# Kernel optimization log

Hardware: AMD Instinct MI355X
Metric: run time of the kernel (lower is better)

Reference implementation:

```python
import jax, jax.numpy as jnp
import numpy as np
from jax import lax

BN_EPS = 1e-5


def _conv(x, w, b):
    # 3x3 conv, stride 1, padding 1 (SAME), NCHW/OIHW
    y = lax.conv_general_dilated(x, w, (1, 1), 'SAME',
                                 dimension_numbers=('NCHW', 'OIHW', 'NCHW'))
    return y + b[None, :, None, None]


def _bn(x, g, b, m, v):
    # eval-mode batchnorm with running stats
    scale = (g / jnp.sqrt(v + BN_EPS))[None, :, None, None]
    return (x - m[None, :, None, None]) * scale + b[None, :, None, None]


def _pool(x):
    # MaxPool2d(2,2), VALID (floor division of spatial dims)
    return lax.reduce_window(x, -jnp.inf, lax.max, (1, 1, 2, 2), (1, 1, 2, 2), 'VALID')


def _quantum(xq, qp):
    """Batched 5-qubit statevector sim of the PennyLane circuit.
    Wire i: RX(xq[:, i%2]) then RY(qp[i%2]); CNOT(0,1); CNOT(1,2); <Z0 Z1>.
    xq: [B, 32] (only first 2 features used). Returns [B] float32.
    """
    B = xq.shape[0]
    psi = jnp.zeros((B, 32), jnp.complex64).at[:, 0].set(1.0)
    for i in range(5):  # fixed tiny loop over wires
        a = xq[:, i % 2]          # [B] data angle
        th = qp[i % 2]            # scalar weight angle
        ca, sa = jnp.cos(a * 0.5), jnp.sin(a * 0.5)
        RX = jnp.stack([jnp.stack([ca, -1j * sa], -1),
                        jnp.stack([-1j * sa, ca], -1)], -2).astype(jnp.complex64)  # [B,2,2]
        cb, sb = jnp.cos(th * 0.5), jnp.sin(th * 0.5)
        RY = jnp.stack([jnp.stack([cb, -sb]), jnp.stack([sb, cb])]).astype(jnp.complex64)  # [2,2]
        U = jnp.einsum('ij,bjk->bik', RY, RX)  # [B,2,2] per-wire unitary
        psi = psi.reshape(B, 2 ** i, 2, 2 ** (4 - i))
        psi = jnp.einsum('bij,bajc->baic', U, psi).reshape(B, 32)
    psi = psi.reshape(B, 2, 2, 2, 2, 2)
    # CNOT(0,1): flip qubit 1 where qubit 0 == 1
    psi = psi.at[:, 1].set(psi[:, 1, ::-1])
    # CNOT(1,2): flip qubit 2 where qubit 1 == 1
    psi = psi.at[:, :, 1].set(psi[:, :, 1, ::-1])
    z01 = jnp.array([[1.0, -1.0], [-1.0, 1.0]], jnp.float32).reshape(1, 2, 2, 1, 1, 1)
    prob = jnp.real(psi) ** 2 + jnp.imag(psi) ** 2
    return jnp.sum(prob * z01, axis=(1, 2, 3, 4, 5))


def setup_inputs() -> dict:
    key = jax.random.key(0)
    ks = jax.random.split(key, 24)
    B = 8192
    s = 0.05
    d = {}
    d['x'] = jax.random.normal(ks[0], (B, 1, 28, 28), jnp.float32)
    d['conv1_w'] = jax.random.normal(ks[1], (64, 1, 3, 3), jnp.float32) * s
    d['conv1_b'] = jax.random.normal(ks[2], (64,), jnp.float32) * s
    d['conv2_w'] = jax.random.normal(ks[3], (128, 64, 3, 3), jnp.float32) * s
    d['conv2_b'] = jax.random.normal(ks[4], (128,), jnp.float32) * s
    d['conv3_w'] = jax.random.normal(ks[5], (256, 128, 3, 3), jnp.float32) * s
    d['conv3_b'] = jax.random.normal(ks[6], (256,), jnp.float32) * s
    for i, c in [(1, 64), (2, 128), (3, 256)]:
        d[f'bn{i}_g'] = jnp.ones((c,), jnp.float32)
        d[f'bn{i}_b'] = jnp.zeros((c,), jnp.float32)
        d[f'bn{i}_m'] = jax.random.normal(ks[6 + i], (c,), jnp.float32) * 0.1
        d[f'bn{i}_v'] = jax.random.uniform(ks[9 + i], (c,), jnp.float32, 0.5, 1.5)
    d['fc1_w'] = jax.random.normal(ks[13], (32, 256 * 3 * 3), jnp.float32) * s
    d['fc1_b'] = jax.random.normal(ks[14], (32,), jnp.float32) * s
    d['q_params'] = jax.random.uniform(ks[15], (8,), jnp.float32)
    d['fc2_w'] = jax.random.normal(ks[16], (128, 1), jnp.float32) * s
    d['fc2_b'] = jax.random.normal(ks[17], (128,), jnp.float32) * s
    d['fc3_w'] = jax.random.normal(ks[18], (2, 128), jnp.float32) * s
    d['fc3_b'] = jax.random.normal(ks[19], (2,), jnp.float32) * s
    return d


def reference(x, conv1_w, conv1_b, conv2_w, conv2_b, conv3_w, conv3_b,
              bn1_g, bn1_b, bn1_m, bn1_v, bn2_g, bn2_b, bn2_m, bn2_v,
              bn3_g, bn3_b, bn3_m, bn3_v, fc1_w, fc1_b, q_params,
              fc2_w, fc2_b, fc3_w, fc3_b):
    h = _pool(jax.nn.relu(_bn(_conv(x, conv1_w, conv1_b), bn1_g, bn1_b, bn1_m, bn1_v)))
    h = _pool(jax.nn.relu(_bn(_conv(h, conv2_w, conv2_b), bn2_g, bn2_b, bn2_m, bn2_v)))
    h = _pool(jax.nn.relu(_bn(_conv(h, conv3_w, conv3_b), bn3_g, bn3_b, bn3_m, bn3_v)))
    # dropout is identity in eval mode
    h = h.reshape(h.shape[0], -1)              # [B, 2304]
    h = h @ fc1_w.T + fc1_b                     # [B, 32]
    q = _quantum(h, q_params)[:, None]          # [B, 1]
    h = q @ fc2_w.T + fc2_b                     # [B, 128]
    logits = h @ fc3_w.T + fc3_b                # [B, 2]
    return jax.nn.log_softmax(logits, axis=1)
```

## Files before the change

kernel.cpp:

```cpp
#include <hip/hip_runtime.h>
#include <hip/hip_bf16.h>
#include <math.h>

typedef float f32x4 __attribute__((ext_vector_type(4)));
typedef float f32x2 __attribute__((ext_vector_type(2)));
typedef short s16x8 __attribute__((ext_vector_type(8)));

static const long long OFF_W2  = 0LL;
static const long long OFF_W3  = 147456LL;
static const long long OFF_AB1 = 737280LL;
static const long long OFF_AB2 = 737792LL;
static const long long OFF_AB3 = 738816LL;
static const long long OFF_Q   = 740864LL;

__device__ inline unsigned short f2bfu(float f) {
    __hip_bfloat16 h = __float2bfloat16(f);
    unsigned short u;
    __builtin_memcpy(&u, &h, 2);
    return u;
}

__global__ __launch_bounds__(256) void prep_k(
    const float* __restrict__ c2w, const float* __restrict__ c3w,
    const float* __restrict__ c1b, const float* __restrict__ g1, const float* __restrict__ b1,
    const float* __restrict__ m1, const float* __restrict__ v1,
    const float* __restrict__ c2b, const float* __restrict__ g2, const float* __restrict__ b2,
    const float* __restrict__ m2, const float* __restrict__ v2,
    const float* __restrict__ c3b, const float* __restrict__ g3, const float* __restrict__ b3,
    const float* __restrict__ m3, const float* __restrict__ v3,
    const float* __restrict__ fc1b, const float* __restrict__ qp,
    const float* __restrict__ fc2w, const float* __restrict__ fc2b,
    const float* __restrict__ fc3w, const float* __restrict__ fc3b,
    short* __restrict__ wT2, short* __restrict__ wT3,
    float2* __restrict__ ab1, float2* __restrict__ ab2, float2* __restrict__ ab3,
    float* __restrict__ qc)
{
    int tid = blockIdx.x * 256 + threadIdx.x;
    if (tid < 73728) {
        int ic = tid & 63, oc = (tid >> 6) & 127, k = tid >> 13;
        wT2[tid] = (short)f2bfu(c2w[(oc * 64 + ic) * 9 + k]);
    }
    if (tid < 294912) {
        int ic = tid & 127, oc = (tid >> 7) & 255, k = tid >> 15;
        wT3[tid] = (short)f2bfu(c3w[(oc * 128 + ic) * 9 + k]);
    }
    if (tid < 64) {
        float s = g1[tid] / sqrtf(v1[tid] + 1e-5f);
        ab1[tid] = make_float2(s, (c1b[tid] - m1[tid]) * s + b1[tid]);
    } else if (tid < 192) {
        int c = tid - 64;
        float s = g2[c] / sqrtf(v2[c] + 1e-5f);
        ab2[c] = make_float2(s, (c2b[c] - m2[c]) * s + b2[c]);
    } else if (tid < 448) {
        int c = tid - 192;
        float s = g3[c] / sqrtf(v3[c] + 1e-5f);
        ab3[c] = make_float2(s, (c3b[c] - m3[c]) * s + b3[c]);
    } else if (tid == 448) {
        float A0 = 0.f, A1 = 0.f, B0 = 0.f, B1 = 0.f;
        for (int k = 0; k < 128; ++k) {
            float f2 = fc2w[k], fb = fc2b[k];
            A0 += fc3w[k] * f2;        B0 += fc3w[k] * fb;
            A1 += fc3w[128 + k] * f2;  B1 += fc3w[128 + k] * fb;
        }
        qc[0] = A0; qc[1] = A1;
        qc[2] = B0 + fc3b[0]; qc[3] = B1 + fc3b[1];
        qc[4] = cosf(qp[1]);  qc[5] = fc1b[1];
    }
}

__global__ __launch_bounds__(512, 4) void fused_k(
    const float* __restrict__ x, const float* __restrict__ c1w,
    const float2* __restrict__ ab1, const float2* __restrict__ ab2,
    const float2* __restrict__ ab3,
    const short* __restrict__ wT2, const short* __restrict__ wT3,
    const float* __restrict__ fc1w, const float* __restrict__ qc,
    float* __restrict__ out)
{
    __shared__ short xs2[16 * 16 * 64];
    __shared__ short u3[8 * 8 * 128];

    float (*xt)[32] = (float (*)[32])u3;
    short* xs3 = u3;
    float* red = (float*)u3;

    int b = blockIdx.x, t = threadIdx.x;

    for (int i = t; i < 8192; i += 512) ((unsigned*)xs2)[i] = 0u;
    for (int i = t; i < 960;  i += 512) ((unsigned*)u3)[i] = 0u;
    __syncthreads();

    for (int i = t; i < 784; i += 512) xt[i / 28 + 1][i % 28 + 1] = x[b * 784 + i];

    int ocg = t & 15;
    float wr[4][9];
    float2 abr[4];
#pragma unroll
    for (int c = 0; c < 4; ++c) {
#pragma unroll
        for (int k = 0; k < 9; ++k) wr[c][k] = c1w[(ocg * 4 + c) * 9 + k];
        abr[c] = ab1[ocg * 4 + c];
    }
    __syncthreads();

    int posb = t >> 4;
    for (int p = posb; p < 196; p += 32) {
        int py = p / 14, px = p % 14;
        int y0 = 2 * py, x0 = 2 * px;
        float patch[4][4];
#pragma unroll
        for (int i = 0; i < 4; ++i)
#pragma unroll
            for (int j = 0; j < 4; ++j) patch[i][j] = xt[y0 + i][x0 + j];

        unsigned short ub[4];
#pragma unroll
        for (int c = 0; c < 4; ++c) {
            f32x2 r0 = {0.f, 0.f};
            f32x2 r1 = {0.f, 0.f};
#pragma unroll
            for (int ky = 0; ky < 3; ++ky)
#pragma unroll
                for (int kx = 0; kx < 3; ++kx) {
                    float wv = wr[c][ky * 3 + kx];
                    f32x2 p0 = {patch[ky + 0][kx], patch[ky + 0][kx + 1]};
                    f32x2 p1 = {patch[ky + 1][kx], patch[ky + 1][kx + 1]};
                    r0 += p0 * wv;
                    r1 += p1 * wv;
                }
            float aa = abr[c].x, bb = abr[c].y;
            f32x2 s0 = r0 * aa + bb;
            f32x2 s1 = r1 * aa + bb;
            float v = fmaxf(fmaxf(s0.x, s0.y), fmaxf(s1.x, s1.y));
            ub[c] = f2bfu(fmaxf(v, 0.f));
        }
        uint2 pk;
        pk.x = (unsigned)ub[0] | ((unsigned)ub[1] << 16);
        pk.y = (unsigned)ub[2] | ((unsigned)ub[3] << 16);
        int blk = (ocg >> 1) ^ ((px + 1) & 7);
        *(uint2*)&xs2[((((py + 1) * 16) + (px + 1)) * 8 + blk) * 8 + (ocg & 1) * 4] = pk;
    }
    __syncthreads();
    for (int i = t; i < 960; i += 512) {
        int pos = i >> 6, w = i & 63;
        int yy = (pos < 8) ? 0 : pos - 7;
        int xx = (pos < 8) ? pos : 0;
        ((unsigned*)xs3)[(yy * 8 + xx) * 64 + w] = 0u;
    }

    int lane = t & 63, wid = t >> 6;
    int quad = lane >> 4, n16 = lane & 15;
    int dy = n16 >> 3, lx = n16 & 7;

    {
        f32x4 acc[14];
        f32x4 z = {0.f, 0.f, 0.f, 0.f};
#pragma unroll
        for (int nt = 0; nt < 14; ++nt) acc[nt] = z;

        const short* pA_base = wT2 + (wid * 16 + n16) * 64 + quad * 8;

#pragma unroll 1
        for (int kykx = 0; kykx < 9; ++kykx) {
            int ky = kykx / 3, kx = kykx - 3 * ky;
            int dyky = dy + ky;
            int xc0 = lx + kx;
            int xc1 = xc0 + 8; if (xc1 > 15) xc1 = 15;
            const short* pA = pA_base + kykx * 8192;
#pragma unroll
            for (int kk = 0; kk < 2; ++kk) {
                s16x8 A = *(const s16x8*)(pA + kk * 32);
                int bi = kk * 4 + quad;
                int blk0 = bi ^ (xc0 & 7);
                int blk1 = bi ^ (xc1 & 7);
                const short* pB0 = &xs2[((dyky * 16 + xc0) * 8 + blk0) * 8];
                const short* pB1 = &xs2[((dyky * 16 + xc1) * 8 + blk1) * 8];
#pragma unroll
                for (int ry = 0; ry < 7; ++ry) {
                    s16x8 B0 = *(const s16x8*)(pB0 + ry * 2048);
                    s16x8 B1 = *(const s16x8*)(pB1 + ry * 2048);
                    acc[2 * ry + 0] = __builtin_amdgcn_mfma_f32_16x16x32_bf16(A, B0, acc[2 * ry + 0], 0, 0, 0);
                    acc[2 * ry + 1] = __builtin_amdgcn_mfma_f32_16x16x32_bf16(A, B1, acc[2 * ry + 1], 0, 0, 0);
                }
            }
        }

        int m = lx >> 1;
        bool keep = (dy == 0) && ((lx & 1) == 0);
        int oc0 = wid * 16 + quad * 4;
        float2 abv[4];
#pragma unroll
        for (int r = 0; r < 4; ++r) abv[r] = ab2[oc0 + r];
#pragma unroll
        for (int nt = 0; nt < 14; ++nt) {
            int ry = nt >> 1, cb = nt & 1;
            int xp = cb * 4 + m;
            float pv[4];
#pragma unroll
            for (int r = 0; r < 4; ++r) {
                float v = acc[nt][r] * abv[r].x + abv[r].y;
                v = fmaxf(v, __shfl_xor(v, 1));
                v = fmaxf(v, __shfl_xor(v, 8));
                pv[r] = fmaxf(v, 0.f);
            }
            if (keep && xp < 7) {
                uint2 pk;
                pk.x = (unsigned)f2bfu(pv[0]) | ((unsigned)f2bfu(pv[1]) << 16);
                pk.y = (unsigned)f2bfu(pv[2]) | ((unsigned)f2bfu(pv[3]) << 16);
                int blk3 = (oc0 >> 3) ^ (((xp + 1) & 7) << 1);
                *(uint2*)&xs3[(((ry + 1) * 8 + (xp + 1)) * 16 + blk3) * 8 + (oc0 & 7)] = pk;
            }
        }
    }
    __syncthreads();

    f32x4 acc[2][3];
    f32x4 z = {0.f, 0.f, 0.f, 0.f};
#pragma unroll
    for (int ml = 0; ml < 2; ++ml)
#pragma unroll
        for (int nt = 0; nt < 3; ++nt) acc[ml][nt] = z;

    const short* pW_base = wT3 + (wid * 32 + n16) * 128 + quad * 8;

#pragma unroll 1
    for (int kykx = 0; kykx < 9; ++kykx) {
        int ky = kykx / 3, kx = kykx - 3 * ky;
        int dyky = dy + ky;
        int x_in = lx + kx; if (x_in > 7) x_in = 7;
        const short* pW0 = pW_base + kykx * 32768;
        const short* pW1 = pW0 + 2048;
#pragma unroll
        for (int kk = 0; kk < 4; ++kk) {
            s16x8 A0 = *(const s16x8*)(pW0 + kk * 32);
            s16x8 A1 = *(const s16x8*)(pW1 + kk * 32);
            int bi = kk * 4 + quad;
            int blk = bi ^ ((x_in & 7) << 1);
            const short* pB = &xs3[((dyky * 8 + x_in) * 16 + blk) * 8];
#pragma unroll
            for (int nt = 0; nt < 3; ++nt) {
                s16x8 B = *(const s16x8*)(pB + nt * 2048);
                acc[0][nt] = __builtin_amdgcn_mfma_f32_16x16x32_bf16(A0, B, acc[0][nt], 0, 0, 0);
                acc[1][nt] = __builtin_amdgcn_mfma_f32_16x16x32_bf16(A1, B, acc[1][nt], 0, 0, 0);
            }
        }
    }
    __syncthreads();

    float vacc = 0.f;
    int m = lx >> 1;
    bool keep = (dy == 0) && ((lx & 1) == 0) && (m < 3);
    const float* fc1w1 = fc1w + 2304;
#pragma unroll
    for (int ml = 0; ml < 2; ++ml) {
        int oc0 = (wid * 2 + ml) * 16 + quad * 4;
        float2 abv[4];
#pragma unroll
        for (int r = 0; r < 4; ++r) abv[r] = ab3[oc0 + r];
#pragma unroll
        for (int nt = 0; nt < 3; ++nt) {
#pragma unroll
            for (int r = 0; r < 4; ++r) {
                float v = acc[ml][nt][r] * abv[r].x + abv[r].y;
                v = fmaxf(v, __shfl_xor(v, 1));
                v = fmaxf(v, __shfl_xor(v, 8));
                v = fmaxf(v, 0.f);
                if (keep) vacc += v * fc1w1[(oc0 + r) * 9 + nt * 3 + m];
            }
        }
    }
#pragma unroll
    for (int s = 1; s < 64; s <<= 1) vacc += __shfl_xor(vacc, s);
    if (lane == 0) red[wid] = vacc;
    __syncthreads();
    if (t == 0) {
        float v = red[0] + red[1] + red[2] + red[3]
                + red[4] + red[5] + red[6] + red[7] + qc[5];
        float q = cosf(v) * qc[4];
        float l0 = q * qc[0] + qc[2];
        float l1 = q * qc[1] + qc[3];
        float mx = fmaxf(l0, l1);
        float lse = mx + logf(__expf(l0 - mx) + __expf(l1 - mx));
        out[b * 2 + 0] = l0 - lse;
        out[b * 2 + 1] = l1 - lse;
    }
}

extern "C" void kernel_launch(void* const* d_in, const int* in_sizes, int n_in,
                              void* d_out, int out_size, void* d_ws, size_t ws_size,
                              hipStream_t stream)
{
    const float* x    = (const float*)d_in[0];
    const float* c1w  = (const float*)d_in[1];
    const float* c1b  = (const float*)d_in[2];
    const float* c2w  = (const float*)d_in[3];
    const float* c2b  = (const float*)d_in[4];
    const float* c3w  = (const float*)d_in[5];
    const float* c3b  = (const float*)d_in[6];
    const float* g1   = (const float*)d_in[7];
    const float* b1   = (const float*)d_in[8];
    const float* m1   = (const float*)d_in[9];
    const float* v1   = (const float*)d_in[10];
    const float* g2   = (const float*)d_in[11];
    const float* b2   = (const float*)d_in[12];
    const float* m2   = (const float*)d_in[13];
    const float* v2   = (const float*)d_in[14];
    const float* g3   = (const float*)d_in[15];
    const float* b3   = (const float*)d_in[16];
    const float* m3   = (const float*)d_in[17];
    const float* v3   = (const float*)d_in[18];
    const float* fc1w = (const float*)d_in[19];
    const float* fc1b = (const float*)d_in[20];
    const float* qp   = (const float*)d_in[21];
    const float* fc2w = (const float*)d_in[22];
    const float* fc2b = (const float*)d_in[23];
    const float* fc3w = (const float*)d_in[24];
    const float* fc3b = (const float*)d_in[25];
    float* out = (float*)d_out;
    char* ws = (char*)d_ws;

    short*  wT2 = (short*)(ws + OFF_W2);
    short*  wT3 = (short*)(ws + OFF_W3);
    float2* ab1 = (float2*)(ws + OFF_AB1);
    float2* ab2 = (float2*)(ws + OFF_AB2);
    float2* ab3 = (float2*)(ws + OFF_AB3);
    float*  qc  = (float*)(ws + OFF_Q);

    int B = in_sizes[0] / 784;

    prep_k<<<1152, 256, 0, stream>>>(c2w, c3w, c1b, g1, b1, m1, v1,
                                     c2b, g2, b2, m2, v2, c3b, g3, b3, m3, v3,
                                     fc1b, qp, fc2w, fc2b, fc3w, fc3b,
                                     wT2, wT3, ab1, ab2, ab3, qc);
    fused_k<<<B, 512, 0, stream>>>(x, c1w, ab1, ab2, ab3, wT2, wT3, fc1w, qc, out);
}
```

Baseline: 963.4 us.

## Switch conv2/conv3 to 32x32x16 MFMA with pool-window-grouped output tiles

Rewrites the conv2 and conv3 implicit-GEMM inner loops to use 32x32x16 bf16 MFMA instead of 16x16x32. The N dimension is remapped so each group of 4 lanes covers one 2x2 pooling window, which lets max-pool use shfl_xor 1 and 2 and skips output rows that pooling would discard. The aim is fewer MFMA issues, fewer LDS B-fragment loads and less wasted compute on padded positions. The cost is more complex indexing, larger accumulator register use and some clamped duplicate positions.

```diff
diff --git a/kernel.cpp b/kernel.cpp
--- a/kernel.cpp
+++ b/kernel.cpp
@@ -2,9 +2,10 @@
 #include <hip/hip_bf16.h>
 #include <math.h>
 
-typedef float f32x4 __attribute__((ext_vector_type(4)));
-typedef float f32x2 __attribute__((ext_vector_type(2)));
-typedef short s16x8 __attribute__((ext_vector_type(8)));
+typedef float f32x4  __attribute__((ext_vector_type(4)));
+typedef float f32x2  __attribute__((ext_vector_type(2)));
+typedef float f32x16 __attribute__((ext_vector_type(16)));
+typedef short s16x8  __attribute__((ext_vector_type(8)));
 
 static const long long OFF_W2  = 0LL;
 static const long long OFF_W3  = 147456LL;
@@ -148,123 +149,144 @@
     }
 
     int lane = t & 63, wid = t >> 6;
-    int quad = lane >> 4, n16 = lane & 15;
-    int dy = n16 >> 3, lx = n16 & 7;
+    int col = lane & 31, hi = lane >> 5;
 
     {
-        f32x4 acc[14];
-        f32x4 z = {0.f, 0.f, 0.f, 0.f};
-#pragma unroll
-        for (int nt = 0; nt < 14; ++nt) acc[nt] = z;
-
-        const short* pA_base = wT2 + (wid * 16 + n16) * 64 + quad * 8;
+        int ocT = wid & 3, ph = wid >> 2;
+        f32x16 acc[4];
+        int py_[4], px_[4];
+#pragma unroll
+        for (int tt = 0; tt < 4; ++tt) {
+#pragma unroll
+            for (int j = 0; j < 16; ++j) acc[tt][j] = 0.f;
+            int T = ph ? (4 + tt) : tt;
+            int Q = T * 7 + (col >> 2); if (Q > 48) Q = 48;
+            int qy = Q / 7, qx = Q - 7 * qy;
+            py_[tt] = 2 * qy + ((col >> 1) & 1);
+            px_[tt] = 2 * qx + (col & 1);
+        }
+
+        const short* pA0 = wT2 + (ocT * 32 + col) * 64 + hi * 8;
 
 #pragma unroll 1
         for (int kykx = 0; kykx < 9; ++kykx) {
             int ky = kykx / 3, kx = kykx - 3 * ky;
-            int dyky = dy + ky;
-            int xc0 = lx + kx;
-            int xc1 = xc0 + 8; if (xc1 > 15) xc1 = 15;
-            const short* pA = pA_base + kykx * 8192;
-#pragma unroll
-            for (int kk = 0; kk < 2; ++kk) {
-                s16x8 A = *(const s16x8*)(pA + kk * 32);
-                int bi = kk * 4 + quad;
-                int blk0 = bi ^ (xc0 & 7);
-                int blk1 = bi ^ (xc1 & 7);
-                const short* pB0 = &xs2[((dyky * 16 + xc0) * 8 + blk0) * 8];
-                const short* pB1 = &xs2[((dyky * 16 + xc1) * 8 + blk1) * 8];
-#pragma unroll
-                for (int ry = 0; ry < 7; ++ry) {
-                    s16x8 B0 = *(const s16x8*)(pB0 + ry * 2048);
-                    s16x8 B1 = *(const s16x8*)(pB1 + ry * 2048);
-                    acc[2 * ry + 0] = __builtin_amdgcn_mfma_f32_16x16x32_bf16(A, B0, acc[2 * ry + 0], 0, 0, 0);
-                    acc[2 * ry + 1] = __builtin_amdgcn_mfma_f32_16x16x32_bf16(A, B1, acc[2 * ry + 1], 0, 0, 0);
+            const short* pA = pA0 + kykx * 8192;
+            int rb[4], e[4];
+#pragma unroll
+            for (int tt = 0; tt < 4; ++tt) {
+                int Y = py_[tt] + ky, X = px_[tt] + kx;
+                rb[tt] = (Y * 16 + X) * 64;
+                e[tt] = X & 7;
+            }
+#pragma unroll
+            for (int sb = 0; sb < 4; sb += 2) {
+                s16x8 A0 = *(const s16x8*)(pA + sb * 16);
+                s16x8 A1 = *(const s16x8*)(pA + sb * 16 + 16);
+#pragma unroll
+                for (int tt = 0; tt < 4; ++tt) {
+                    s16x8 B0 = *(const s16x8*)&xs2[rb[tt] + (((sb * 2 + hi) ^ e[tt]) << 3)];
+                    acc[tt] = __builtin_amdgcn_mfma_f32_32x32x16_bf16(A0, B0, acc[tt], 0, 0, 0);
+                    s16x8 B1 = *(const s16x8*)&xs2[rb[tt] + ((((sb + 1) * 2 + hi) ^ e[tt]) << 3)];
+                    acc[tt] = __builtin_amdgcn_mfma_f32_32x32x16_bf16(A1, B1, acc[tt], 0, 0, 0);
                 }
             }
         }
 
-        int m = lx >> 1;
-        bool keep = (dy == 0) && ((lx & 1) == 0);
-        int oc0 = wid * 16 + quad * 4;
-        float2 abv[4];
-#pragma unroll
-        for (int r = 0; r < 4; ++r) abv[r] = ab2[oc0 + r];
-#pragma unroll
-        for (int nt = 0; nt < 14; ++nt) {
-            int ry = nt >> 1, cb = nt & 1;
-            int xp = cb * 4 + m;
-            float pv[4];
-#pragma unroll
-            for (int r = 0; r < 4; ++r) {
-                float v = acc[nt][r] * abv[r].x + abv[r].y;
-                v = fmaxf(v, __shfl_xor(v, 1));
-                v = fmaxf(v, __shfl_xor(v, 8));
-                pv[r] = fmaxf(v, 0.f);
-            }
-            if (keep && xp < 7) {
-                uint2 pk;
-                pk.x = (unsigned)f2bfu(pv[0]) | ((unsigned)f2bfu(pv[1]) << 16);
-                pk.y = (unsigned)f2bfu(pv[2]) | ((unsigned)f2bfu(pv[3]) << 16);
-                int blk3 = (oc0 >> 3) ^ (((xp + 1) & 7) << 1);
-                *(uint2*)&xs3[(((ry + 1) * 8 + (xp + 1)) * 16 + blk3) * 8 + (oc0 & 7)] = pk;
-            }
-        }
-    }
-    __syncthreads();
-
-    f32x4 acc[2][3];
-    f32x4 z = {0.f, 0.f, 0.f, 0.f};
-#pragma unroll
-    for (int ml = 0; ml < 2; ++ml)
-#pragma unroll
-        for (int nt = 0; nt < 3; ++nt) acc[ml][nt] = z;
-
-    const short* pW_base = wT3 + (wid * 32 + n16) * 128 + quad * 8;
+        bool wact = ((col & 3) == 0) && (col < 28);
+#pragma unroll
+        for (int tt = 0; tt < 4; ++tt) {
+            if (tt < 3 || ph == 0) {
+                int qy = py_[tt] >> 1, qx = px_[tt] >> 1;
+                int wb = ((qy + 1) * 8 + (qx + 1)) * 16;
+                int sw = ((qx + 1) & 7) << 1;
+#pragma unroll
+                for (int g = 0; g < 4; ++g) {
+                    int oc0 = ocT * 32 + 4 * hi + 8 * g;
+                    float2 ab[4];
+#pragma unroll
+                    for (int j = 0; j < 4; ++j) ab[j] = ab2[oc0 + j];
+                    unsigned short us[4];
+#pragma unroll
+                    for (int j = 0; j < 4; ++j) {
+                        float v = acc[tt][g * 4 + j] * ab[j].x + ab[j].y;
+                        v = fmaxf(v, __shfl_xor(v, 1));
+                        v = fmaxf(v, __shfl_xor(v, 2));
+                        us[j] = f2bfu(fmaxf(v, 0.f));
+                    }
+                    if (wact) {
+                        uint2 pk;
+                        pk.x = (unsigned)us[0] | ((unsigned)us[1] << 16);
+                        pk.y = (unsigned)us[2] | ((unsigned)us[3] << 16);
+                        int blk3 = (oc0 >> 3) ^ sw;
+                        *(uint2*)&xs3[(wb + blk3) * 8 + (oc0 & 7)] = pk;
+                    }
+                }
+            }
+        }
+    }
+    __syncthreads();
+
+    f32x16 c3[2];
+    int py3_[2], px3_[2];
+#pragma unroll
+    for (int tt = 0; tt < 2; ++tt) {
+#pragma unroll
+        for (int j = 0; j < 16; ++j) c3[tt][j] = 0.f;
+        int q = tt * 8 + (col >> 2); if (q > 8) q = 8;
+        int qy = q / 3, qx = q - 3 * qy;
+        py3_[tt] = 2 * qy + ((col >> 1) & 1);
+        px3_[tt] = 2 * qx + (col & 1);
+    }
+    const short* pW0 = wT3 + (wid * 32 + col) * 128 + hi * 8;
 
 #pragma unroll 1
     for (int kykx = 0; kykx < 9; ++kykx) {
         int ky = kykx / 3, kx = kykx - 3 * ky;
-        int dyky = dy + ky;
-        int x_in = lx + kx; if (x_in > 7) x_in = 7;
-        const short* pW0 = pW_base + kykx * 32768;
-        const short* pW1 = pW0 + 2048;
-#pragma unroll
-        for (int kk = 0; kk < 4; ++kk) {
-            s16x8 A0 = *(const s16x8*)(pW0 + kk * 32);
-            s16x8 A1 = *(const s16x8*)(pW1 + kk * 32);
-            int bi = kk * 4 + quad;
-            int blk = bi ^ ((x_in & 7) << 1);
-            const short* pB = &xs3[((dyky * 8 + x_in) * 16 + blk) * 8];
-#pragma unroll
-            for (int nt = 0; nt < 3; ++nt) {
-                s16x8 B = *(const s16x8*)(pB + nt * 2048);
-                acc[0][nt] = __builtin_amdgcn_mfma_f32_16x16x32_bf16(A0, B, acc[0][nt], 0, 0, 0);
-                acc[1][nt] = __builtin_amdgcn_mfma_f32_16x16x32_bf16(A1, B, acc[1][nt], 0, 0, 0);
+        const short* pW = pW0 + kykx * 32768;
+        int rb0 = ((py3_[0] + ky) * 8 + (px3_[0] + kx)) * 128;
+        int e0 = ((px3_[0] + kx) & 7) << 1;
+        int rb1 = ((py3_[1] + ky) * 8 + (px3_[1] + kx)) * 128;
+        int e1 = ((px3_[1] + kx) & 7) << 1;
+#pragma unroll
+        for (int sb = 0; sb < 8; sb += 4) {
+            s16x8 A0 = *(const s16x8*)(pW + (sb + 0) * 16);
+            s16x8 A1 = *(const s16x8*)(pW + (sb + 1) * 16);
+            s16x8 A2 = *(const s16x8*)(pW + (sb + 2) * 16);
+            s16x8 A3 = *(const s16x8*)(pW + (sb + 3) * 16);
+#pragma unroll
+            for (int ss = 0; ss < 4; ++ss) {
+                s16x8 Af = (ss == 0) ? A0 : (ss == 1) ? A1 : (ss == 2) ? A2 : A3;
+                int o = (sb + ss) * 2 + hi;
+                s16x8 B0 = *(const s16x8*)&xs3[rb0 + ((o ^ e0) << 3)];
+                c3[0] = __builtin_amdgcn_mfma_f32_32x32x16_bf16(Af, B0, c3[0], 0, 0, 0);
+                s16x8 B1 = *(const s16x8*)&xs3[rb1 + ((o ^ e1) << 3)];
+                c3[1] = __builtin_amdgcn_mfma_f32_32x32x16_bf16(Af, B1, c3[1], 0, 0, 0);
             }
         }
     }
     __syncthreads();
 
     float vacc = 0.f;
-    int m = lx >> 1;
-    bool keep = (dy == 0) && ((lx & 1) == 0) && (m < 3);
     const float* fc1w1 = fc1w + 2304;
 #pragma unroll
-    for (int ml = 0; ml < 2; ++ml) {
-        int oc0 = (wid * 2 + ml) * 16 + quad * 4;
-        float2 abv[4];
-#pragma unroll
-        for (int r = 0; r < 4; ++r) abv[r] = ab3[oc0 + r];
-#pragma unroll
-        for (int nt = 0; nt < 3; ++nt) {
-#pragma unroll
-            for (int r = 0; r < 4; ++r) {
-                float v = acc[ml][nt][r] * abv[r].x + abv[r].y;
+    for (int tt = 0; tt < 2; ++tt) {
+        int qy = py3_[tt] >> 1, qx = px3_[tt] >> 1;
+        bool act = ((col & 3) == 0) && (tt == 0 || col == 0);
+        int fidx = qy * 3 + qx;
+#pragma unroll
+        for (int g = 0; g < 4; ++g) {
+            int oc0 = wid * 32 + 4 * hi + 8 * g;
+            float2 ab[4];
+#pragma unroll
+            for (int j = 0; j < 4; ++j) ab[j] = ab3[oc0 + j];
+#pragma unroll
+            for (int j = 0; j < 4; ++j) {
+                float v = c3[tt][g * 4 + j] * ab[j].x + ab[j].y;
                 v = fmaxf(v, __shfl_xor(v, 1));
-                v = fmaxf(v, __shfl_xor(v, 8));
+                v = fmaxf(v, __shfl_xor(v, 2));
                 v = fmaxf(v, 0.f);
-                if (keep) vacc += v * fc1w1[(oc0 + r) * 9 + nt * 3 + m];
+                if (act) vacc += v * fc1w1[(oc0 + j) * 9 + fidx];
             }
         }
     }
```

After: 1.063 ms. 1.1x slower.
